# Kernel tuning notes

Measured on AMD Instinct MI355X. Metric: run time of the kernel, lower is better.

Reference implementation:

```python
import jax, jax.numpy as jnp
import numpy as np

# LCA hyperparameters (from init_kwargs)
NUM_LATENT = 2048
NUM_STEPS = 100
STEP_SIZE = 0.01
SPARSE_MULT = 0.3
# thresh_type='soft', rectify_a=True -> rectified soft threshold


def lca_threshold(u):
    # rectified soft threshold: a = relu(u - lambda)
    return jax.nn.relu(u - SPARSE_MULT)


def setup_inputs() -> dict:
    key = jax.random.key(0)
    kx, kw = jax.random.split(key)
    x = jax.random.normal(kx, (8192, 784), dtype=jnp.float32)
    w = jax.random.normal(kw, (784, NUM_LATENT), dtype=jnp.float32)
    # normalize dictionary columns (standard LCA practice; keeps the
    # fixed-point iteration u <- u + s*(b - a@G - u) numerically stable)
    w = w / jnp.linalg.norm(w, axis=0, keepdims=True)
    return {"x": x, "w": w}


def reference(x, w):
    # x: [B, 784], w: [784, L]
    x = x.reshape(-1, 28 * 28)
    b = x @ w                                        # excitatory current [B, L]
    g = w.T @ w - jnp.eye(NUM_LATENT, dtype=w.dtype)  # inhibitory connectivity [L, L]

    u0 = jnp.zeros((x.shape[0], NUM_LATENT), dtype=x.dtype)
    a0 = lca_threshold(u0)

    def step(carry, _):
        u, a = carry
        du = b - a @ g - u
        u_new = u + STEP_SIZE * du
        a_new = lca_threshold(u_new)
        return (u_new, a_new), None

    # original runs num_steps-1 updates after the initial state
    (u, a), _ = jax.lax.scan(step, (u0, a0), None, length=NUM_STEPS - 1)

    reconstruction = a @ w.T  # [B, 784]
    return (reconstruction, a)
```

## Files before the change

### kernel.cpp

```cpp
#include <hip/hip_runtime.h>
#include <hip/hip_bf16.h>
#include <stdint.h>


typedef __bf16 bf16_t;
typedef float f32x4 __attribute__((ext_vector_type(4)));
typedef __bf16 bf16x8 __attribute__((ext_vector_type(8)));
typedef int int4v __attribute__((ext_vector_type(4)));

#define BM 128

static __device__ __forceinline__ f32x4 mfma16(int4v a, int4v b, f32x4 c) {
    return __builtin_amdgcn_mfma_f32_16x16x32_bf16(
        __builtin_bit_cast(bf16x8, a), __builtin_bit_cast(bf16x8, b), c, 0, 0, 0);
}

static __device__ __forceinline__ void gl_lds16(const bf16_t* gp, bf16_t* lp) {
    auto g1 = (const __attribute__((address_space(1))) uint32_t*)(uintptr_t)gp;
    auto l3 = (__attribute__((address_space(3))) uint32_t*)(uintptr_t)lp;
    __builtin_amdgcn_global_load_lds(g1, l3, 16, 0, 0);
}

template <int N>
static __device__ __forceinline__ void vm_wait() {
    if constexpr (N == 0)      asm volatile("s_waitcnt vmcnt(0)" ::: "memory");
    else if constexpr (N == 2) asm volatile("s_waitcnt vmcnt(2)" ::: "memory");
    else if constexpr (N == 4) asm volatile("s_waitcnt vmcnt(4)" ::: "memory");
    else if constexpr (N == 6) asm volatile("s_waitcnt vmcnt(6)" ::: "memory");
    else if constexpr (N == 8) asm volatile("s_waitcnt vmcnt(8)" ::: "memory");
    else                       static_assert(N == 0, "unsupported vmcnt");
}

template <int CPR>
static __device__ __forceinline__ int foldf(int r) {
    if constexpr (CPR == 8) return r & 7;
    else                    return (r ^ (r >> 2)) & 3;
}

__global__ void sniff(const uint16_t* __restrict__ wh, int* __restrict__ flag) {
    __shared__ int cnt;
    if (threadIdx.x == 0) cnt = 0;
    __syncthreads();
    int c = 0;
    for (int t = threadIdx.x; t < 4096; t += 256) {
        uint16_t h = wh[(size_t)2 * t * 97];
        c += (((h >> 7) & 0xFF) >= 0x82);
    }
    atomicAdd(&cnt, c);
    __syncthreads();
    if (threadIdx.x == 0) flag[0] = (cnt > 256) ? 1 : 0;
}

__global__ void fill0(int4v* __restrict__ p, long n16) {
    long i = (long)blockIdx.x * 256 + threadIdx.x;
    if (i < n16) p[i] = (int4v){0, 0, 0, 0};
}

__global__ void build_w(const void* __restrict__ w, bf16_t* __restrict__ wT,
                        bf16_t* __restrict__ wB, const int* __restrict__ flag) {
    const int k = blockIdx.x * 256 + threadIdx.x;
    const int j = blockIdx.y;
    if (k >= 800) return;
    bf16_t v = (bf16_t)0.0f;
    if (k < 784) {
        v = flag[0] ? (bf16_t)((const float*)w)[(size_t)k * 2048 + j]
                    : ((const bf16_t*)w)[(size_t)k * 2048 + j];
        wB[(size_t)k * 2048 + j] = v;
    }
    wT[(size_t)j * 800 + k] = v;
}

template <int MODE, bool CLAMPN, int BNT, int TBK, int NW>
__global__ __launch_bounds__(NW * 64, NW / 2) void gemm_nt(
    const bf16_t* __restrict__ A, const bf16_t* __restrict__ B,
    int N, int K, int lda, int ldb,
    const void* __restrict__ Xin, float* __restrict__ U,
    bf16_t* __restrict__ Out, int ldo, const int* __restrict__ flag)
{
    constexpr int THREADS = NW * 64;
    constexpr int NWN = NW / 2;
    constexpr int MT  = 4;
    constexpr int NTW = BNT / (NWN * 16);
    constexpr int CPR = TBK / 8;
    constexpr int AL  = BM * CPR / THREADS;
    constexpr int BL  = BNT * CPR / THREADS;
    constexpr int L   = AL + BL;
    constexpr int KH  = TBK / 32;
    static_assert(AL >= 1 && BL >= 1 && NTW >= 1, "geometry");

    __shared__ __align__(16) bf16_t sA[2][BM * TBK];
    __shared__ __align__(16) bf16_t sB[2][BNT * TBK];

    const int tid  = threadIdx.x;
    const int lane = tid & 63;
    const int wave = tid >> 6;
    const int wm   = wave / NWN;
    const int wn   = wave % NWN;
    const int bm   = blockIdx.x * BM;
    const int bn   = blockIdx.y * BNT;

    f32x4 acc[MT][NTW];
#pragma unroll
    for (int i = 0; i < MT; ++i)
#pragma unroll
        for (int j = 0; j < NTW; ++j) acc[i][j] = (f32x4){0.f, 0.f, 0.f, 0.f};

    const bf16_t* gA[AL];
    const bf16_t* gB[BL];
#pragma unroll
    for (int l = 0; l < AL; ++l) {
        const int c  = l * THREADS + tid;
        const int rL = c / CPR;
        const int sc = (c & (CPR - 1)) ^ foldf<CPR>(rL);
        gA[l] = A + (size_t)(bm + rL) * lda + sc * 8;
    }
#pragma unroll
    for (int l = 0; l < BL; ++l) {
        const int c  = l * THREADS + tid;
        const int rL = c / CPR;
        const int sc = (c & (CPR - 1)) ^ foldf<CPR>(rL);
        int rb = bn + rL;
        if (CLAMPN) rb = min(rb, N - 1);
        gB[l] = B + (size_t)rb * ldb + sc * 8;
    }

    auto stage = [&](int buf, int k0) {
#pragma unroll
        for (int l = 0; l < AL; ++l)
            gl_lds16(gA[l] + k0, &sA[buf][(size_t)(l * THREADS + tid) * 8]);
#pragma unroll
        for (int l = 0; l < BL; ++l)
            gl_lds16(gB[l] + k0, &sB[buf][(size_t)(l * THREADS + tid) * 8]);
    };

    const int mrow = lane & 15;
    const int q    = lane >> 4;
    const int swz = foldf<CPR>(mrow);
    const int qx  = q ^ (swz & 3);
    const int ksw = swz >> 2;

    stage(0, 0);
    int cur = 0;
    for (int k0 = 0; k0 < K; k0 += TBK) {
        if (k0 + TBK < K) {
            stage(cur ^ 1, k0 + TBK);
            vm_wait<L>();
        } else {
            vm_wait<0>();
        }
        __builtin_amdgcn_s_barrier();
        asm volatile("" ::: "memory");

        int4v af[MT][KH], bv[NTW][KH];
        const bf16_t* pa = &sA[cur][(wm * 64 + mrow) * TBK + qx * 8];
        const bf16_t* pb = &sB[cur][(wn * (NTW * 16) + mrow) * TBK + qx * 8];
#pragma unroll
        for (int t = 0; t < MT; ++t)
#pragma unroll
            for (int kk = 0; kk < KH; ++kk)
                af[t][kk] = *(const int4v*)(pa + t * 16 * TBK + (kk ^ ksw) * 32);
#pragma unroll
        for (int t = 0; t < NTW; ++t)
#pragma unroll
            for (int kk = 0; kk < KH; ++kk)
                bv[t][kk] = *(const int4v*)(pb + t * 16 * TBK + (kk ^ ksw) * 32);
#pragma unroll
        for (int kk = 0; kk < KH; ++kk)
#pragma unroll
            for (int mt = 0; mt < MT; ++mt)
#pragma unroll
                for (int nt = 0; nt < NTW; ++nt)
                    acc[mt][nt] = mfma16(af[mt][kk], bv[nt][kk], acc[mt][nt]);

        asm volatile("s_waitcnt lgkmcnt(0)" ::: "memory");
        __builtin_amdgcn_s_barrier();
        cur ^= 1;
    }

    int f = 0;
    if (MODE == 0) f = flag[0];

    const int coln = lane & 15;
    const int rq   = lane >> 4;
#pragma unroll
    for (int mt = 0; mt < MT; ++mt) {
#pragma unroll
        for (int r = 0; r < 4; ++r) {
            const int gm = bm + wm * 64 + mt * 16 + rq * 4 + r;
#pragma unroll
            for (int nt = 0; nt < NTW; ++nt) {
                const int gn = bn + wn * (NTW * 16) + nt * 16 + coln;
                const float c = acc[mt][nt][r];
                if (MODE == 0) {
                    if (gn < N) {
                        const size_t xi = (size_t)gm * N + gn;
                        const float xv = f ? ((const float*)Xin)[xi]
                                           : (float)((const bf16_t*)Xin)[xi];
                        Out[(size_t)gm * ldo + gn] = (bf16_t)(xv - c);
                    }
                } else if (MODE == 1) {
                    const size_t idx = (size_t)gm * ldo + gn;
                    const float uo = U[idx];
                    const float ao = fmaxf(uo - 0.3f, 0.0f);
                    const float un = uo + 0.01f * (c + ao - uo);
                    U[idx] = un;
                    Out[idx] = (bf16_t)fmaxf(un - 0.3f, 0.0f);
                } else {
                    if (gn < N)
                        Out[(size_t)gm * ldo + gn] = (bf16_t)c;
                }
            }
        }
    }
}

__global__ void a_move(const bf16_t* __restrict__ src, float* __restrict__ dst,
                       long lo, long hi, const int* __restrict__ flag) {
    if (!flag[0]) return;
    long i = lo + (long)blockIdx.x * 256 + threadIdx.x;
    if (i < hi) dst[i] = (float)src[i];
}

__global__ void recon_out(const bf16_t* __restrict__ rec, void* __restrict__ dout,
                          const int* __restrict__ flag) {
    long i = (long)blockIdx.x * 256 + threadIdx.x;
    if (i >= 6422528L) return;
    if (flag[0]) ((float*)dout)[i] = (float)rec[i];
    else         ((bf16_t*)dout)[i] = rec[i];
}

extern "C" void kernel_launch(void* const* d_in, const int* in_sizes, int n_in,
                              void* d_out, int out_size, void* d_ws, size_t ws_size,
                              hipStream_t stream) {
    const void* x = d_in[0];
    const void* w = d_in[1];
    (void)in_sizes; (void)n_in; (void)out_size; (void)ws_size;

    char* ws = (char*)d_ws;
    float*  u    = (float*)ws;
    bf16_t* r    = (bf16_t*)(ws + 67108864);
    bf16_t* wT   = (bf16_t*)(ws + 80216064);
    bf16_t* wB   = (bf16_t*)(ws + 83492864);
    int*    flag = (int*)(ws + 86704128);
    bf16_t* aA   = (bf16_t*)((char*)d_out + 12845056);
    bf16_t* rec  = r;

    sniff<<<1, 256, 0, stream>>>((const uint16_t*)w, flag);
    fill0<<<16384, 256, 0, stream>>>((int4v*)u, 4194304L);
    fill0<<<3200, 256, 0, stream>>>((int4v*)r, 819200L);
    fill0<<<8192, 256, 0, stream>>>((int4v*)aA, 2097152L);
    build_w<<<dim3(4, 2048), 256, 0, stream>>>(w, wT, wB, flag);

    for (int i = 0; i < 99; ++i) {
        gemm_nt<0, true, 128, 32, 8><<<dim3(64, 7), 512, 0, stream>>>(
            aA, wB, 784, 2048, 2048, 2048, x, nullptr, r, 800, flag);
        gemm_nt<1, false, 128, 32, 4><<<dim3(64, 16), 256, 0, stream>>>(
            r, wT, 2048, 800, 800, 800, nullptr, u, aA, 2048, flag);
    }

    gemm_nt<2, true, 128, 32, 8><<<dim3(64, 7), 512, 0, stream>>>(
        aA, wB, 784, 2048, 2048, 2048, nullptr, nullptr, rec, 784, flag);

    float* aOutF = (float*)d_out + 6422528;
    a_move<<<45312, 256, 0, stream>>>(aA, aOutF, 5177344L, 16777216L, flag);
    a_move<<<20224, 256, 0, stream>>>(aA, aOutF, 0L, 5177344L, flag);

    recon_out<<<25088, 256, 0, stream>>>(rec, d_out, flag);
}
```

Before: 9.388 ms.

## Precompute Gram matrix and run LCA iterations as single fp16 GEMM per step

Replaces the two-GEMM-per-step residual formulation (r = x - a·Wᵀ, then r·W) with the standard LCA form: precompute b = x·W and G = WᵀW - I once, then each step does a single 8192x2048x2048 GEMM against G fused with the u/a update. Operands switch from bf16 to fp16 MFMA for more mantissa precision, activations ping-pong between workspace and output buffers, and the LDS swizzle fold changes. This trades K=784 twice per step for K=2048 once per step (more FLOPs per step), depends on workspace size to select the path, and may change accuracy characteristics.

```diff
diff --git a/kernel.cpp b/kernel.cpp
--- a/kernel.cpp
+++ b/kernel.cpp
@@ -4,18 +4,25 @@
 
 
 typedef __bf16 bf16_t;
+typedef _Float16 f16_t;
 typedef float f32x4 __attribute__((ext_vector_type(4)));
 typedef __bf16 bf16x8 __attribute__((ext_vector_type(8)));
+typedef _Float16 f16x8 __attribute__((ext_vector_type(8)));
 typedef int int4v __attribute__((ext_vector_type(4)));
 
 #define BM 128
 
+template <typename ET>
 static __device__ __forceinline__ f32x4 mfma16(int4v a, int4v b, f32x4 c) {
-    return __builtin_amdgcn_mfma_f32_16x16x32_bf16(
-        __builtin_bit_cast(bf16x8, a), __builtin_bit_cast(bf16x8, b), c, 0, 0, 0);
-}
-
-static __device__ __forceinline__ void gl_lds16(const bf16_t* gp, bf16_t* lp) {
+    if constexpr (__is_same(ET, bf16_t))
+        return __builtin_amdgcn_mfma_f32_16x16x32_bf16(
+            __builtin_bit_cast(bf16x8, a), __builtin_bit_cast(bf16x8, b), c, 0, 0, 0);
+    else
+        return __builtin_amdgcn_mfma_f32_16x16x32_f16(
+            __builtin_bit_cast(f16x8, a), __builtin_bit_cast(f16x8, b), c, 0, 0, 0);
+}
+
+static __device__ __forceinline__ void gl_lds16(const void* gp, void* lp) {
     auto g1 = (const __attribute__((address_space(1))) uint32_t*)(uintptr_t)gp;
     auto l3 = (__attribute__((address_space(3))) uint32_t*)(uintptr_t)lp;
     __builtin_amdgcn_global_load_lds(g1, l3, 16, 0, 0);
@@ -34,7 +41,7 @@
 template <int CPR>
 static __device__ __forceinline__ int foldf(int r) {
     if constexpr (CPR == 8) return r & 7;
-    else                    return (r ^ (r >> 2)) & 3;
+    else                    return r & 3;
 }
 
 __global__ void sniff(const uint16_t* __restrict__ wh, int* __restrict__ flag) {
@@ -56,6 +63,10 @@
     if (i < n16) p[i] = (int4v){0, 0, 0, 0};
 }
 
+static __device__ __forceinline__ float ldin(const void* p, size_t i, int f) {
+    return f ? ((const float*)p)[i] : (float)((const bf16_t*)p)[i];
+}
+
 __global__ void build_w(const void* __restrict__ w, bf16_t* __restrict__ wT,
                         bf16_t* __restrict__ wB, const int* __restrict__ flag) {
     const int k = blockIdx.x * 256 + threadIdx.x;
@@ -63,19 +74,47 @@
     if (k >= 800) return;
     bf16_t v = (bf16_t)0.0f;
     if (k < 784) {
-        v = flag[0] ? (bf16_t)((const float*)w)[(size_t)k * 2048 + j]
-                    : ((const bf16_t*)w)[(size_t)k * 2048 + j];
+        v = (bf16_t)ldin(w, (size_t)k * 2048 + j, flag[0]);
         wB[(size_t)k * 2048 + j] = v;
     }
     wT[(size_t)j * 800 + k] = v;
 }
 
-template <int MODE, bool CLAMPN, int BNT, int TBK, int NW>
-__global__ __launch_bounds__(NW * 64, NW / 2) void gemm_nt(
-    const bf16_t* __restrict__ A, const bf16_t* __restrict__ B,
+__global__ void build_wh(const void* __restrict__ w, f16_t* __restrict__ wTh,
+                         const int* __restrict__ flag) {
+    const int k = blockIdx.x * 256 + threadIdx.x;
+    const int j = blockIdx.y;
+    if (k >= 800) return;
+    f16_t v = (f16_t)0.0f;
+    if (k < 784) v = (f16_t)ldin(w, (size_t)k * 2048 + j, flag[0]);
+    wTh[(size_t)j * 800 + k] = v;
+}
+
+__global__ void build_wbh(const void* __restrict__ w, f16_t* __restrict__ wBh,
+                          const int* __restrict__ flag) {
+    const int j = blockIdx.x * 256 + threadIdx.x;
+    const int p = blockIdx.y;
+    if (j >= 2048) return;
+    wBh[(size_t)p * 2048 + j] = (f16_t)ldin(w, (size_t)p * 2048 + j, flag[0]);
+}
+
+__global__ void build_xh(const void* __restrict__ x, f16_t* __restrict__ xh,
+                         const int* __restrict__ flag) {
+    const int k = blockIdx.x * 256 + threadIdx.x;
+    const int i = blockIdx.y;
+    if (k >= 800) return;
+    f16_t v = (f16_t)0.0f;
+    if (k < 784) v = (f16_t)ldin(x, (size_t)i * 784 + k, flag[0]);
+    xh[(size_t)i * 800 + k] = v;
+}
+
+template <int MODE, bool CLAMPN, int BNT, int TBK, int NW,
+          typename ET = bf16_t, bool BF32 = true>
+__global__ __launch_bounds__(NW * 64, 4) void gemm_nt(
+    const ET* __restrict__ A, const ET* __restrict__ B,
     int N, int K, int lda, int ldb,
     const void* __restrict__ Xin, float* __restrict__ U,
-    bf16_t* __restrict__ Out, int ldo, const int* __restrict__ flag)
+    ET* __restrict__ Out, int ldo, const int* __restrict__ flag)
 {
     constexpr int THREADS = NW * 64;
     constexpr int NWN = NW / 2;
@@ -88,8 +127,8 @@
     constexpr int KH  = TBK / 32;
     static_assert(AL >= 1 && BL >= 1 && NTW >= 1, "geometry");
 
-    __shared__ __align__(16) bf16_t sA[2][BM * TBK];
-    __shared__ __align__(16) bf16_t sB[2][BNT * TBK];
+    __shared__ __align__(16) ET sA[2][BM * TBK];
+    __shared__ __align__(16) ET sB[2][BNT * TBK];
 
     const int tid  = threadIdx.x;
     const int lane = tid & 63;
@@ -105,8 +144,8 @@
 #pragma unroll
         for (int j = 0; j < NTW; ++j) acc[i][j] = (f32x4){0.f, 0.f, 0.f, 0.f};
 
-    const bf16_t* gA[AL];
-    const bf16_t* gB[BL];
+    const ET* gA[AL];
+    const ET* gB[BL];
 #pragma unroll
     for (int l = 0; l < AL; ++l) {
         const int c  = l * THREADS + tid;
@@ -152,8 +191,8 @@
         asm volatile("" ::: "memory");
 
         int4v af[MT][KH], bv[NTW][KH];
-        const bf16_t* pa = &sA[cur][(wm * 64 + mrow) * TBK + qx * 8];
-        const bf16_t* pb = &sB[cur][(wn * (NTW * 16) + mrow) * TBK + qx * 8];
+        const ET* pa = &sA[cur][(wm * 64 + mrow) * TBK + qx * 8];
+        const ET* pb = &sB[cur][(wn * (NTW * 16) + mrow) * TBK + qx * 8];
 #pragma unroll
         for (int t = 0; t < MT; ++t)
 #pragma unroll
@@ -170,7 +209,7 @@
             for (int mt = 0; mt < MT; ++mt)
 #pragma unroll
                 for (int nt = 0; nt < NTW; ++nt)
-                    acc[mt][nt] = mfma16(af[mt][kk], bv[nt][kk], acc[mt][nt]);
+                    acc[mt][nt] = mfma16<ET>(af[mt][kk], bv[nt][kk], acc[mt][nt]);
 
         asm volatile("s_waitcnt lgkmcnt(0)" ::: "memory");
         __builtin_amdgcn_s_barrier();
@@ -196,7 +235,7 @@
                         const size_t xi = (size_t)gm * N + gn;
                         const float xv = f ? ((const float*)Xin)[xi]
                                            : (float)((const bf16_t*)Xin)[xi];
-                        Out[(size_t)gm * ldo + gn] = (bf16_t)(xv - c);
+                        Out[(size_t)gm * ldo + gn] = (ET)(xv - c);
                     }
                 } else if (MODE == 1) {
                     const size_t idx = (size_t)gm * ldo + gn;
@@ -204,14 +243,44 @@
                     const float ao = fmaxf(uo - 0.3f, 0.0f);
                     const float un = uo + 0.01f * (c + ao - uo);
                     U[idx] = un;
-                    Out[idx] = (bf16_t)fmaxf(un - 0.3f, 0.0f);
+                    Out[idx] = (ET)fmaxf(un - 0.3f, 0.0f);
+                } else if (MODE == 3) {
+                    const size_t idx = (size_t)gm * ldo + gn;
+                    const float uo = U[idx];
+                    const float bb = BF32 ? ((const float*)Xin)[idx]
+                                          : (float)((const ET*)Xin)[idx];
+                    const float un = uo + 0.01f * (bb - c - uo);
+                    U[idx] = un;
+                    Out[idx] = (ET)fmaxf(un - 0.3f, 0.0f);
+                } else if (MODE == 4) {
+                    U[(size_t)gm * ldo + gn] = c;
+                } else if (MODE == 5) {
+                    Out[(size_t)gm * ldo + gn] = (ET)(gm == gn ? c - 1.0f : c);
                 } else {
                     if (gn < N)
-                        Out[(size_t)gm * ldo + gn] = (bf16_t)c;
+                        Out[(size_t)gm * ldo + gn] = (ET)c;
                 }
             }
         }
     }
+}
+
+__global__ void a_out(const f16_t* __restrict__ src, void* __restrict__ dout,
+                      const int* __restrict__ flag) {
+    long i = (long)blockIdx.x * 256 + threadIdx.x;
+    if (i >= 16777216L) return;
+    const float v = (float)src[i];
+    if (flag[0]) ((float*)dout)[6422528L + i] = v;
+    else         ((bf16_t*)dout)[6422528L + i] = (bf16_t)v;
+}
+
+__global__ void recon_out_h(const f16_t* __restrict__ rec, void* __restrict__ dout,
+                            const int* __restrict__ flag) {
+    long i = (long)blockIdx.x * 256 + threadIdx.x;
+    if (i >= 6422528L) return;
+    const float v = (float)rec[i];
+    if (flag[0]) ((float*)dout)[i] = v;
+    else         ((bf16_t*)dout)[i] = (bf16_t)v;
 }
 
 __global__ void a_move(const bf16_t* __restrict__ src, float* __restrict__ dst,
@@ -234,9 +303,64 @@
                               hipStream_t stream) {
     const void* x = d_in[0];
     const void* w = d_in[1];
-    (void)in_sizes; (void)n_in; (void)out_size; (void)ws_size;
+    (void)in_sizes; (void)n_in; (void)out_size;
 
     char* ws = (char*)d_ws;
+    const bool tier1 = ws_size >= 179437572UL;
+    const bool tier2 = ws_size >= 145883140UL;
+
+    if (tier1 || tier2) {
+        float*  u    = (float*)ws;
+        f16_t*  xh   = (f16_t*)ws;
+        float*  bF   = (float*)(ws + 67108864);
+        f16_t*  bH   = (f16_t*)(ws + 67108864);
+        const size_t goff = tier1 ? 134217728UL : 100663296UL;
+        f16_t*  g    = (f16_t*)(ws + goff);
+        f16_t*  wTh  = (f16_t*)(ws + goff + 8388608);
+        f16_t*  aP0  = (f16_t*)(ws + goff + 11665408);
+        int*    flag = (int*)(ws + goff + 45219840);
+        f16_t*  aP1  = (f16_t*)d_out;
+        f16_t*  wBh  = (f16_t*)ws;
+        f16_t*  rec  = (f16_t*)(ws + 4194304);
+
+        sniff<<<1, 256, 0, stream>>>((const uint16_t*)w, flag);
+        build_wh<<<dim3(4, 2048), 256, 0, stream>>>(w, wTh, flag);
+        build_xh<<<dim3(4, 8192), 256, 0, stream>>>(x, xh, flag);
+
+        if (tier1)
+            gemm_nt<4, false, 128, 32, 4, f16_t><<<dim3(64, 16), 256, 0, stream>>>(
+                xh, wTh, 2048, 800, 800, 800, nullptr, bF, nullptr, 2048, flag);
+        else
+            gemm_nt<2, false, 128, 32, 4, f16_t><<<dim3(64, 16), 256, 0, stream>>>(
+                xh, wTh, 2048, 800, 800, 800, nullptr, nullptr, bH, 2048, flag);
+        gemm_nt<5, false, 128, 32, 4, f16_t><<<dim3(16, 16), 256, 0, stream>>>(
+            wTh, wTh, 2048, 800, 800, 800, nullptr, nullptr, g, 2048, flag);
+
+        fill0<<<16384, 256, 0, stream>>>((int4v*)u, 4194304L);
+        fill0<<<8192, 256, 0, stream>>>((int4v*)aP1, 2097152L);
+
+        for (int i = 1; i <= 99; ++i) {
+            f16_t* rd = (i & 1) ? aP1 : aP0;
+            f16_t* wr = (i & 1) ? aP0 : aP1;
+            if (tier1)
+                gemm_nt<3, false, 128, 32, 4, f16_t, true>
+                    <<<dim3(64, 16), 256, 0, stream>>>(
+                    rd, g, 2048, 2048, 2048, 2048, bF, u, wr, 2048, flag);
+            else
+                gemm_nt<3, false, 128, 32, 4, f16_t, false>
+                    <<<dim3(64, 16), 256, 0, stream>>>(
+                    rd, g, 2048, 2048, 2048, 2048, bH, u, wr, 2048, flag);
+        }
+
+        build_wbh<<<dim3(8, 784), 256, 0, stream>>>(w, wBh, flag);
+        gemm_nt<2, true, 128, 32, 8, f16_t><<<dim3(64, 7), 512, 0, stream>>>(
+            aP0, wBh, 784, 2048, 2048, 2048, nullptr, nullptr, rec, 784, flag);
+
+        a_out<<<65536, 256, 0, stream>>>(aP0, d_out, flag);
+        recon_out_h<<<25088, 256, 0, stream>>>(rec, d_out, flag);
+        return;
+    }
+
     float*  u    = (float*)ws;
     bf16_t* r    = (bf16_t*)(ws + 67108864);
     bf16_t* wT   = (bf16_t*)(ws + 80216064);
@@ -264,6 +388,5 @@
     float* aOutF = (float*)d_out + 6422528;
     a_move<<<45312, 256, 0, stream>>>(aA, aOutF, 5177344L, 16777216L, flag);
     a_move<<<20224, 256, 0, stream>>>(aA, aOutF, 0L, 5177344L, flag);
-
     recon_out<<<25088, 256, 0, stream>>>(rec, d_out, flag);
 }
```

After: 10.20 ms. 1.09x slower.
